# Kernel optimization log

Hardware: AMD Instinct MI355X
Metric: run time of the kernel (lower is better)

Reference implementation:

```python
import jax, jax.numpy as jnp
import numpy as np

N, E, H, NODE_IN, EDGE_DIM, L = 10000, 400000, 128, 6, 3, 4
LN_EPS = 1e-5


def _lin_init(key, fan_in, fan_out):
    return jax.random.normal(key, (fan_in, fan_out), dtype=jnp.float32) / np.sqrt(fan_in)


def setup_inputs() -> dict:
    key = jax.random.key(0)
    ks = jax.random.split(key, 24)
    x = jax.random.normal(ks[0], (N, NODE_IN), dtype=jnp.float32)
    edge_index = jax.random.randint(ks[1], (2, E), 0, N, dtype=jnp.int64)
    edge_attr = jax.random.normal(ks[2], (E, EDGE_DIM), dtype=jnp.float32)
    # encoder
    enc_w1 = _lin_init(ks[3], NODE_IN, H); enc_b1 = jnp.zeros((H,), jnp.float32)
    enc_w2 = _lin_init(ks[4], H, H); enc_b2 = jnp.zeros((H,), jnp.float32)
    # per-layer stacked params [L, ...]
    msg_w1 = jax.vmap(lambda k: _lin_init(k, 2 * H + EDGE_DIM, H))(jax.random.split(ks[5], L))
    msg_b1 = jnp.zeros((L, H), jnp.float32)
    msg_w2 = jax.vmap(lambda k: _lin_init(k, H, H))(jax.random.split(ks[6], L))
    msg_b2 = jnp.zeros((L, H), jnp.float32)
    upd_w1 = jax.vmap(lambda k: _lin_init(k, 2 * H, H))(jax.random.split(ks[7], L))
    upd_b1 = jnp.zeros((L, H), jnp.float32)
    upd_w2 = jax.vmap(lambda k: _lin_init(k, H, H))(jax.random.split(ks[8], L))
    upd_b2 = jnp.zeros((L, H), jnp.float32)
    ln_g = jnp.ones((L, H), jnp.float32)
    ln_b = jnp.zeros((L, H), jnp.float32)
    # decoder
    dec_w1 = _lin_init(ks[9], H, H); dec_b1 = jnp.zeros((H,), jnp.float32)
    dec_w2 = _lin_init(ks[10], H, 1); dec_b2 = jnp.zeros((1,), jnp.float32)
    return dict(x=x, edge_index=edge_index, edge_attr=edge_attr,
                enc_w1=enc_w1, enc_b1=enc_b1, enc_w2=enc_w2, enc_b2=enc_b2,
                msg_w1=msg_w1, msg_b1=msg_b1, msg_w2=msg_w2, msg_b2=msg_b2,
                upd_w1=upd_w1, upd_b1=upd_b1, upd_w2=upd_w2, upd_b2=upd_b2,
                ln_g=ln_g, ln_b=ln_b,
                dec_w1=dec_w1, dec_b1=dec_b1, dec_w2=dec_w2, dec_b2=dec_b2)


def _layernorm(h, g, b):
    mu = jnp.mean(h, axis=-1, keepdims=True)
    var = jnp.mean(jnp.square(h - mu), axis=-1, keepdims=True)
    return (h - mu) * jax.lax.rsqrt(var + LN_EPS) * g + b


def reference(x, edge_index, edge_attr,
              enc_w1, enc_b1, enc_w2, enc_b2,
              msg_w1, msg_b1, msg_w2, msg_b2,
              upd_w1, upd_b1, upd_w2, upd_b2,
              ln_g, ln_b,
              dec_w1, dec_b1, dec_w2, dec_b2):
    src, tgt = edge_index[0], edge_index[1]  # PyG default flow: message from x_j=src to x_i=tgt
    # in-degree counts for mean aggregation (zero-degree nodes -> 0 output, like scatter_mean)
    counts = jax.ops.segment_sum(jnp.ones((E,), jnp.float32), tgt, num_segments=N)
    inv_counts = (1.0 / jnp.maximum(counts, 1.0))[:, None]
    # encoder
    h = jax.nn.relu(x @ enc_w1 + enc_b1) @ enc_w2 + enc_b2  # [N, H]
    for l in range(L):
        x_i = h[tgt]  # [E, H] target features
        x_j = h[src]  # [E, H] source features
        m_in = jnp.concatenate([x_i, x_j, edge_attr], axis=-1)  # [E, 2H+edge_dim]
        m = jax.nn.relu(m_in @ msg_w1[l] + msg_b1[l]) @ msg_w2[l] + msg_b2[l]  # [E, H]
        agg = jax.ops.segment_sum(m, tgt, num_segments=N) * inv_counts  # [N, H] mean aggregate
        u_in = jnp.concatenate([h, agg], axis=-1)  # [N, 2H]
        u = jax.nn.relu(u_in @ upd_w1[l] + upd_b1[l]) @ upd_w2[l] + upd_b2[l]
        h = _layernorm(u + h, ln_g[l], ln_b[l])  # residual (in==out channels)
    # decoder
    return jax.nn.relu(h @ dec_w1 + dec_b1) @ dec_w2 + dec_b2  # [N, 1]
```

## Files before the change

kernel.cpp:

```cpp
#include <hip/hip_runtime.h>

#define NN 10000
#define NE 400000
#define HD 128
#define NIN 6
#define EDIM 3
#define NL 4
#define CAP 96
#define LN_EPS 1e-5f

typedef unsigned short u16;
using short8 = __attribute__((ext_vector_type(8))) short;
using f32x4 = __attribute__((ext_vector_type(4))) float;

__device__ __forceinline__ u16 f2bf(float x) {
    unsigned u = __float_as_uint(x);
    return (u16)((u + 0x7fff + ((u >> 16) & 1)) >> 16);
}
__device__ __forceinline__ float bf2f(u16 h) { return __uint_as_float(((unsigned)h) << 16); }
__device__ __forceinline__ void split2(float x, u16& hi, u16& lo) {
    hi = f2bf(x);
    lo = f2bf(x - bf2f(hi));
}
#define MFMA(a, b, c) __builtin_amdgcn_mfma_f32_16x16x32_bf16((a), (b), (c), 0, 0, 0)


__global__ __launch_bounds__(256) void k_prep(const float* __restrict__ msg_w2, const float* __restrict__ msg_b2,
                                              const float* __restrict__ upd_w1, float* __restrict__ M2,
                                              float* __restrict__ c2, int* __restrict__ cnt) {
    int idx = blockIdx.x * 256 + threadIdx.x;
    if (idx < 65536) {
        int l = idx >> 14, rem = idx & 16383, i = rem >> 7, jj = rem & 127;
        const float* U1b = upd_w1 + (size_t)l * 2 * HD * HD + (size_t)HD * HD;
        const float* W2 = msg_w2 + (size_t)l * HD * HD + (size_t)i * HD;
        float acc = 0.f;
        for (int t = 0; t < HD; ++t) acc += W2[t] * U1b[(size_t)t * HD + jj];
        M2[idx] = acc;
    } else if (idx < 66048) {
        int r = idx - 65536;
        int l = r >> 7, jj = r & 127;
        const float* U1b = upd_w1 + (size_t)l * 2 * HD * HD + (size_t)HD * HD;
        const float* b2 = msg_b2 + l * HD;
        float acc = 0.f;
        for (int t = 0; t < HD; ++t) acc += b2[t] * U1b[(size_t)t * HD + jj];
        c2[r] = acc;
    } else if (idx < 76048) {
        cnt[idx - 66048] = 0;
    }
}


__global__ __launch_bounds__(256) void k_frag(const float* __restrict__ upd_w1, const float* __restrict__ M2,
                                              const float* __restrict__ upd_w2, const float* __restrict__ msg_w1,
                                              const float* __restrict__ dec_w1, const float* __restrict__ enc_w2,
                                              u16* __restrict__ fG1, u16* __restrict__ fG2, u16* __restrict__ fPQ,
                                              u16* __restrict__ fDec, u16* __restrict__ fEnc) {
    int g = blockIdx.x * 256 + threadIdx.x;
    if (g < 16384) {
        int l = g >> 12, r = g & 4095;
        int ct = r >> 9, ks = (r >> 6) & 7, lane = r & 63;
        int n = ct * 16 + (lane & 15), kb = ks * 32 + ((lane >> 4) << 3);
        u16* dst = fG1 + (size_t)g * 8;
        const float* U = upd_w1 + (size_t)l * 256 * 128;
        const float* Ml = M2 + (size_t)l * 128 * 128;
#pragma unroll
        for (int j = 0; j < 8; ++j) {
            int k = kb + j;
            float v = (k < 128) ? U[(size_t)k * 128 + n] : Ml[(size_t)(k - 128) * 128 + n];
            dst[j] = f2bf(v);
        }
    } else if (g < 24576) {
        int gg = g - 16384;
        int l = gg >> 11, r = gg & 2047;
        int ct = r >> 8, ks = (r >> 6) & 3, lane = r & 63;
        int n = ct * 16 + (lane & 15), kb = ks * 32 + ((lane >> 4) << 3);
        u16* dst = fG2 + (size_t)gg * 8;
        const float* W = upd_w2 + (size_t)l * 128 * 128;
#pragma unroll
        for (int j = 0; j < 8; ++j) dst[j] = f2bf(W[(size_t)(kb + j) * 128 + n]);
    } else if (g < 40960) {
        int gg = g - 24576;
        int li = gg >> 12, r = gg & 4095;
        int ct = r >> 8, ks = (r >> 6) & 3, lane = r & 63;
        int n = ct * 16 + (lane & 15), kb = ks * 32 + ((lane >> 4) << 3);
        u16* dst = fPQ + (size_t)gg * 8;
        const float* W = msg_w1 + (size_t)li * (2 * HD + EDIM) * HD;
#pragma unroll
        for (int j = 0; j < 8; ++j) {
            int k = kb + j;
            float v = (n < 128) ? W[(size_t)k * 128 + n] : W[(size_t)(128 + k) * 128 + (n - 128)];
            dst[j] = f2bf(v);
        }
    } else if (g < 43008) {
        int r = g - 40960;
        int ct = r >> 8, ks = (r >> 6) & 3, lane = r & 63;
        int n = ct * 16 + (lane & 15), kb = ks * 32 + ((lane >> 4) << 3);
        u16* dst = fDec + (size_t)r * 8;
#pragma unroll
        for (int j = 0; j < 8; ++j) dst[j] = f2bf(dec_w1[(size_t)(kb + j) * 128 + n]);
    } else if (g < 45056) {
        int r = g - 43008;
        int ct = r >> 8, ks = (r >> 6) & 3, lane = r & 63;
        int n = ct * 16 + (lane & 15), kb = ks * 32 + ((lane >> 4) << 3);
        u16* dst = fEnc + (size_t)r * 8;
#pragma unroll
        for (int j = 0; j < 8; ++j) dst[j] = f2bf(enc_w2[(size_t)(kb + j) * 128 + n]);
    }
}


__global__ __launch_bounds__(256) void k_scatter(const int* __restrict__ src, const int* __restrict__ tgt,
                                                 const float* __restrict__ ea, int* __restrict__ cnt,
                                                 float4* __restrict__ sea) {
    int e = blockIdx.x * 256 + threadIdx.x;
    if (e >= NE) return;
    int t = tgt[e];
    int pos = atomicAdd(&cnt[t], 1);
    if (pos < CAP) {
        sea[t * CAP + pos] =
            make_float4(ea[e * 3], ea[e * 3 + 1], ea[e * 3 + 2], __uint_as_float((unsigned)src[e]));
    }
}


__global__ __launch_bounds__(512) void k_enc(const float* __restrict__ x, const float* __restrict__ ew1,
                                             const float* __restrict__ eb1, const u16* __restrict__ fEnc,
                                             const float* __restrict__ eb2, const u16* __restrict__ fPQ0,
                                             const float* __restrict__ mb1, u16* __restrict__ h_hi,
                                             u16* __restrict__ h_lo, float* __restrict__ PQf,
                                             u16* __restrict__ Qb) {
    __shared__ u16 tHi[2048], tLo[2048];
    int tid = threadIdx.x, w = tid >> 6, lane = tid & 63, q = lane >> 4, c = lane & 15;
    int band = blockIdx.x * 16;
    {
        int col = w * 16 + c;
        float wv[NIN];
#pragma unroll
        for (int k = 0; k < NIN; ++k) wv[k] = ew1[k * HD + col];
        float ebv = eb1[col];
#pragma unroll
        for (int reg = 0; reg < 4; ++reg) {
            int row = band + q * 4 + reg;
            float t = ebv;
#pragma unroll
            for (int k = 0; k < NIN; ++k) t += x[(size_t)row * NIN + k] * wv[k];
            t = fmaxf(t, 0.f);
            u16 hi, lo;
            split2(t, hi, lo);
            int r16 = q * 4 + reg;
            int a = r16 * 128 + (((col >> 3) ^ r16) << 3) + (col & 7);
            tHi[a] = hi;
            tLo[a] = lo;
        }
    }
    __syncthreads();
    short8 aH[4], aL[4];
#pragma unroll
    for (int ks = 0; ks < 4; ++ks) {
        int a = c * 128 + (((ks * 4 + q) ^ c) << 3);
        aH[ks] = *(const short8*)&tHi[a];
        aL[ks] = *(const short8*)&tLo[a];
    }
    f32x4 acc = {0, 0, 0, 0};
    {
        const u16* fb = fEnc + (size_t)w * 4 * 512 + lane * 8;
#pragma unroll
        for (int ks = 0; ks < 4; ++ks) {
            short8 b = *(const short8*)(fb + ks * 512);
            acc = MFMA(aH[ks], b, acc);
            acc = MFMA(aL[ks], b, acc);
        }
    }
    __syncthreads();
    {
        int col = w * 16 + c;
        float ebv = eb2[col];
#pragma unroll
        for (int reg = 0; reg < 4; ++reg) {
            int r16 = q * 4 + reg, row = band + r16;
            float hval = acc[reg] + ebv;
            u16 hi, lo;
            split2(hval, hi, lo);
            h_hi[(size_t)row * HD + col] = hi;
            h_lo[(size_t)row * HD + col] = lo;
            int a = r16 * 128 + (((col >> 3) ^ r16) << 3) + (col & 7);
            tHi[a] = hi;
            tLo[a] = lo;
        }
    }
    __syncthreads();
#pragma unroll
    for (int ks = 0; ks < 4; ++ks) {
        int a = c * 128 + (((ks * 4 + q) ^ c) << 3);
        aH[ks] = *(const short8*)&tHi[a];
        aL[ks] = *(const short8*)&tLo[a];
    }
#pragma unroll
    for (int i = 0; i < 2; ++i) {
        int ctg = w * 2 + i;
        const u16* fb = fPQ0 + (size_t)ctg * 4 * 512 + lane * 8;
        f32x4 a3 = {0, 0, 0, 0};
#pragma unroll
        for (int ks = 0; ks < 4; ++ks) {
            short8 b = *(const short8*)(fb + ks * 512);
            a3 = MFMA(aH[ks], b, a3);
            a3 = MFMA(aL[ks], b, a3);
        }
        int col = ctg * 16 + c;
        if (ctg < 8) {
            float bias = mb1[col];
#pragma unroll
            for (int reg = 0; reg < 4; ++reg)
                PQf[(size_t)(band + q * 4 + reg) * HD + col] = a3[reg] + bias;
        } else {
            int colq = col - 128;
#pragma unroll
            for (int reg = 0; reg < 4; ++reg)
                Qb[(size_t)(band + q * 4 + reg) * HD + colq] = f2bf(a3[reg]);
        }
    }
}


template <bool LAST>
__global__ __launch_bounds__(512) void k_layer(
    const float* __restrict__ PQf_in, const u16* __restrict__ Qb_in,
    const int* __restrict__ cnt, const float4* __restrict__ sea, const float* __restrict__ wc,
    u16* __restrict__ h_hi, u16* __restrict__ h_lo,
    const u16* __restrict__ fG1, const u16* __restrict__ fG2,
    const float* __restrict__ ub1, const float* __restrict__ c2l, const float* __restrict__ ub2,
    const float* __restrict__ g, const float* __restrict__ bb,
    const u16* __restrict__ fPQ, const float* __restrict__ nb1,
    float* __restrict__ PQf_out, u16* __restrict__ Qb_out,
    const u16* __restrict__ fDec, const float* __restrict__ db1, const float* __restrict__ dw2,
    const float* __restrict__ db2, float* __restrict__ out) {
    __shared__ u16 sHi[2048], sLo[2048];
    __shared__ u16 tHi[2048], tLo[2048];
    __shared__ float red[16][8][2];
    int tid = threadIdx.x, w = tid >> 6, lane = tid & 63, q = lane >> 4, c = lane & 15;
    int band = blockIdx.x * 16;
    int j = lane * 2;
    {
        float2 wcr0 = *(const float2*)(wc + j);
        float2 wcr1 = *(const float2*)(wc + HD + j);
        float2 wcr2 = *(const float2*)(wc + 2 * HD + j);
#pragma unroll
        for (int i = 0; i < 2; ++i) {
            int r16 = w * 2 + i;
            int n = __builtin_amdgcn_readfirstlane(band + r16);
            int cn = cnt[n];
            float invn = 1.0f / fmaxf((float)cn, 1.0f);
            int cle = __builtin_amdgcn_readfirstlane(cn < CAP ? cn : CAP);
            float2 p = *(const float2*)(PQf_in + (size_t)n * HD + j);
            float acc0 = 0.f, acc1 = 0.f;
            const float4* bucket = sea + (size_t)n * CAP;
            auto edge1 = [&](float4 A) {
                int sv = (int)__float_as_uint(A.w);
                float c0 = A.x * wcr0.x + A.y * wcr1.x + A.z * wcr2.x;
                float c1 = A.x * wcr0.y + A.y * wcr1.y + A.z * wcr2.y;
                unsigned u = *(const unsigned*)(Qb_in + (size_t)sv * HD + j);
                acc0 += fmaxf(p.x + __uint_as_float(u << 16) + c0, 0.f);
                acc1 += fmaxf(p.y + __uint_as_float(u & 0xffff0000u) + c1, 0.f);
            };
            int e = 0;
            for (; e + 3 < cle; e += 4) {
                float4 A0 = bucket[e], A1 = bucket[e + 1], A2 = bucket[e + 2], A3 = bucket[e + 3];
                edge1(A0);
                edge1(A1);
                edge1(A2);
                edge1(A3);
            }
            for (; e < cle; ++e) edge1(bucket[e]);
            float v0 = acc0 * invn, v1 = acc1 * invn;
            u16 h0, l0, h1, l1;
            split2(v0, h0, l0);
            split2(v1, h1, l1);
            int a = r16 * 128 + (((j >> 3) ^ r16) << 3) + (j & 7);
            *(ushort2*)&sHi[a] = make_ushort2(h0, h1);
            *(ushort2*)&sLo[a] = make_ushort2(l0, l1);
        }
    }
    __syncthreads();
    short8 aH[8], aL[8];
    {
        size_t rb = (size_t)(band + c) * HD + q * 8;
#pragma unroll
        for (int ks = 0; ks < 4; ++ks) {
            aH[ks] = *(const short8*)(h_hi + rb + ks * 32);
            aL[ks] = *(const short8*)(h_lo + rb + ks * 32);
            int a = c * 128 + (((ks * 4 + q) ^ c) << 3);
            aH[4 + ks] = *(const short8*)&sHi[a];
            aL[4 + ks] = *(const short8*)&sLo[a];
        }
    }
    f32x4 acc = {0, 0, 0, 0};
    {
        const u16* fb = fG1 + (size_t)w * 8 * 512 + lane * 8;
#pragma unroll
        for (int ks = 0; ks < 8; ++ks) {
            short8 b = *(const short8*)(fb + ks * 512);
            acc = MFMA(aH[ks], b, acc);
            acc = MFMA(aL[ks], b, acc);
        }
    }
    float alv[4];
#pragma unroll
    for (int reg = 0; reg < 4; ++reg) alv[reg] = (cnt[band + q * 4 + reg] > 0) ? 1.f : 0.f;
    {
        int col = w * 16 + c;
        float u1b = ub1[col], cc = c2l[col];
#pragma unroll
        for (int reg = 0; reg < 4; ++reg) {
            int r16 = q * 4 + reg;
            float t = fmaxf(acc[reg] + u1b + alv[reg] * cc, 0.f);
            u16 hi, lo;
            split2(t, hi, lo);
            int a = r16 * 128 + (((col >> 3) ^ r16) << 3) + (col & 7);
            tHi[a] = hi;
            tLo[a] = lo;
        }
    }
    __syncthreads();
    short8 aH2[4], aL2[4];
#pragma unroll
    for (int ks = 0; ks < 4; ++ks) {
        int a = c * 128 + (((ks * 4 + q) ^ c) << 3);
        aH2[ks] = *(const short8*)&tHi[a];
        aL2[ks] = *(const short8*)&tLo[a];
    }
    f32x4 acc2 = {0, 0, 0, 0};
    {
        const u16* fb = fG2 + (size_t)w * 4 * 512 + lane * 8;
#pragma unroll
        for (int ks = 0; ks < 4; ++ks) {
            short8 b = *(const short8*)(fb + ks * 512);
            acc2 = MFMA(aH2[ks], b, acc2);
            acc2 = MFMA(aL2[ks], b, acc2);
        }
    }
    float vv[4];
    {
        int col = w * 16 + c;
        float u2b = ub2[col];
#pragma unroll
        for (int reg = 0; reg < 4; ++reg) {
            size_t idx = (size_t)(band + q * 4 + reg) * HD + col;
            float hres = bf2f(h_hi[idx]) + bf2f(h_lo[idx]);
            vv[reg] = acc2[reg] + u2b + hres;
        }
    }
#pragma unroll
    for (int reg = 0; reg < 4; ++reg) {
        float s = vv[reg];
        float s2 = vv[reg] * vv[reg];
        for (int m = 1; m < 16; m <<= 1) {
            s += __shfl_xor(s, m);
            s2 += __shfl_xor(s2, m);
        }
        if (c == 0) {
            red[q * 4 + reg][w][0] = s;
            red[q * 4 + reg][w][1] = s2;
        }
    }
    __syncthreads();
    float mu[4], rs[4];
#pragma unroll
    for (int reg = 0; reg < 4; ++reg) {
        int r16 = q * 4 + reg;
        float S1 = 0.f, S2 = 0.f;
#pragma unroll
        for (int ww = 0; ww < 8; ++ww) {
            S1 += red[r16][ww][0];
            S2 += red[r16][ww][1];
        }
        float m = S1 * (1.f / HD);
        float var = S2 * (1.f / HD) - m * m;
        mu[reg] = m;
        rs[reg] = rsqrtf(var + LN_EPS);
    }
    {
        int col = w * 16 + c;
        float gg = g[col], bv = bb[col];
#pragma unroll
        for (int reg = 0; reg < 4; ++reg) {
            int r16 = q * 4 + reg;
            float o = (vv[reg] - mu[reg]) * rs[reg] * gg + bv;
            u16 hi, lo;
            split2(o, hi, lo);
            int a = r16 * 128 + (((col >> 3) ^ r16) << 3) + (col & 7);
            tHi[a] = hi;
            tLo[a] = lo;
            if (!LAST) {
                size_t idx = (size_t)(band + r16) * HD + col;
                h_hi[idx] = hi;
                h_lo[idx] = lo;
            }
        }
    }
    __syncthreads();
    short8 aH3[4], aL3[4];
#pragma unroll
    for (int ks = 0; ks < 4; ++ks) {
        int a = c * 128 + (((ks * 4 + q) ^ c) << 3);
        aH3[ks] = *(const short8*)&tHi[a];
        aL3[ks] = *(const short8*)&tLo[a];
    }
    if (!LAST) {
#pragma unroll
        for (int i = 0; i < 2; ++i) {
            int ctg = w * 2 + i;
            const u16* fb = fPQ + (size_t)ctg * 4 * 512 + lane * 8;
            f32x4 a3 = {0, 0, 0, 0};
#pragma unroll
            for (int ks = 0; ks < 4; ++ks) {
                short8 b = *(const short8*)(fb + ks * 512);
                a3 = MFMA(aH3[ks], b, a3);
                a3 = MFMA(aL3[ks], b, a3);
            }
            int col = ctg * 16 + c;
            if (ctg < 8) {
                float bias = nb1[col];
#pragma unroll
                for (int reg = 0; reg < 4; ++reg)
                    PQf_out[(size_t)(band + q * 4 + reg) * HD + col] = a3[reg] + bias;
            } else {
                int colq = col - 128;
#pragma unroll
                for (int reg = 0; reg < 4; ++reg)
                    Qb_out[(size_t)(band + q * 4 + reg) * HD + colq] = f2bf(a3[reg]);
            }
        }
    } else {
        float part[4];
        {
            const u16* fb = fDec + (size_t)w * 4 * 512 + lane * 8;
            f32x4 a3 = {0, 0, 0, 0};
#pragma unroll
            for (int ks = 0; ks < 4; ++ks) {
                short8 b = *(const short8*)(fb + ks * 512);
                a3 = MFMA(aH3[ks], b, a3);
                a3 = MFMA(aL3[ks], b, a3);
            }
            int col = w * 16 + c;
            float w2v = dw2[col], b1v = db1[col];
#pragma unroll
            for (int reg = 0; reg < 4; ++reg) part[reg] = fmaxf(a3[reg] + b1v, 0.f) * w2v;
        }
#pragma unroll
        for (int reg = 0; reg < 4; ++reg) {
            float s = part[reg];
            for (int m = 1; m < 16; m <<= 1) s += __shfl_xor(s, m);
            if (c == 0) red[q * 4 + reg][w][0] = s;
        }
        __syncthreads();
        if (tid < 16) {
            float s = db2[0];
#pragma unroll
            for (int ww = 0; ww < 8; ++ww) s += red[tid][ww][0];
            out[band + tid] = s;
        }
    }
}


extern "C" void kernel_launch(void* const* d_in, const int* in_sizes, int n_in,
                              void* d_out, int out_size, void* d_ws, size_t ws_size,
                              hipStream_t stream) {
    const float* x = (const float*)d_in[0];
    const int* eidx = (const int*)d_in[1];
    const float* eattr = (const float*)d_in[2];
    const float* enc_w1 = (const float*)d_in[3];
    const float* enc_b1 = (const float*)d_in[4];
    const float* enc_w2 = (const float*)d_in[5];
    const float* enc_b2 = (const float*)d_in[6];
    const float* msg_w1 = (const float*)d_in[7];
    const float* msg_b1 = (const float*)d_in[8];
    const float* msg_w2 = (const float*)d_in[9];
    const float* msg_b2 = (const float*)d_in[10];
    const float* upd_w1 = (const float*)d_in[11];
    const float* upd_b1 = (const float*)d_in[12];
    const float* upd_w2 = (const float*)d_in[13];
    const float* upd_b2 = (const float*)d_in[14];
    const float* ln_g = (const float*)d_in[15];
    const float* ln_b = (const float*)d_in[16];
    const float* dec_w1 = (const float*)d_in[17];
    const float* dec_b1 = (const float*)d_in[18];
    const float* dec_w2 = (const float*)d_in[19];
    const float* dec_b2 = (const float*)d_in[20];
    const int* srcp = eidx;
    const int* tgtp = eidx + NE;

    char* base = (char*)d_ws;
    size_t off = 0;
    auto alloc = [&](size_t bytes) -> void* {
        off = (off + 15) & ~(size_t)15;
        void* p = base + off;
        off += bytes;
        return p;
    };
    float4* sea = (float4*)alloc((size_t)NN * CAP * 16);
    float* PQf0 = (float*)alloc((size_t)NN * HD * 4);
    float* PQf1 = (float*)alloc((size_t)NN * HD * 4);
    u16* Qb0 = (u16*)alloc((size_t)NN * HD * 2);
    u16* Qb1 = (u16*)alloc((size_t)NN * HD * 2);
    u16* h_hi = (u16*)alloc((size_t)NN * HD * 2);
    u16* h_lo = (u16*)alloc((size_t)NN * HD * 2);
    int* cnt = (int*)alloc((size_t)NN * 4);
    float* M2 = (float*)alloc((size_t)NL * HD * HD * 4);
    float* c2 = (float*)alloc((size_t)NL * HD * 4);
    u16* fG1 = (u16*)alloc((size_t)131072 * 2);
    u16* fG2 = (u16*)alloc((size_t)65536 * 2);
    u16* fPQ = (u16*)alloc((size_t)131072 * 2);
    u16* fDec = (u16*)alloc((size_t)16384 * 2);
    u16* fEnc = (u16*)alloc((size_t)16384 * 2);

    k_prep<<<298, 256, 0, stream>>>(msg_w2, msg_b2, upd_w1, M2, c2, cnt);
    k_frag<<<176, 256, 0, stream>>>(upd_w1, M2, upd_w2, msg_w1, dec_w1, enc_w2, fG1, fG2, fPQ, fDec, fEnc);
    k_scatter<<<(NE + 255) / 256, 256, 0, stream>>>(srcp, tgtp, eattr, cnt, sea);
    k_enc<<<NN / 16, 512, 0, stream>>>(x, enc_w1, enc_b1, fEnc, enc_b2, fPQ, msg_b1, h_hi, h_lo, PQf0, Qb0);

    float* PQin = PQf0;
    u16* Qin = Qb0;
    float* PQout = PQf1;
    u16* Qout = Qb1;
    for (int l = 0; l < NL; ++l) {
        const float* wc = msg_w1 + (size_t)l * (2 * HD + EDIM) * HD + (size_t)2 * HD * HD;
        if (l < NL - 1) {
            k_layer<false><<<NN / 16, 512, 0, stream>>>(
                PQin, Qin, cnt, sea, wc, h_hi, h_lo,
                fG1 + (size_t)l * 32768, fG2 + (size_t)l * 16384,
                upd_b1 + l * HD, c2 + l * HD, upd_b2 + l * HD, ln_g + l * HD, ln_b + l * HD,
                fPQ + (size_t)(l + 1) * 32768, msg_b1 + (size_t)(l + 1) * HD, PQout, Qout,
                nullptr, nullptr, nullptr, nullptr, nullptr);
        } else {
            k_layer<true><<<NN / 16, 512, 0, stream>>>(
                PQin, Qin, cnt, sea, wc, h_hi, h_lo,
                fG1 + (size_t)l * 32768, fG2 + (size_t)l * 16384,
                upd_b1 + l * HD, c2 + l * HD, upd_b2 + l * HD, ln_g + l * HD, ln_b + l * HD,
                nullptr, nullptr, nullptr, nullptr,
                fDec, dec_b1, dec_w2, dec_b2, (float*)d_out);
        }
        float* tf = PQin; PQin = PQout; PQout = tf;
        u16* tq = Qin; Qin = Qout; Qout = tq;
    }
}
```

Before: 286.5 us.

## Fuse all stages into one persistent cooperative kernel with grid syncs

Replaces the chain of prep, fragment, scatter, encoder and four layer launches with a single cooperative kernel of 625 blocks that separates stages with grid.sync(). The aim is to remove per-launch overhead and the gaps between the many small kernels. The layer body also streams MFMA A operands instead of holding them all in registers, which lowers register pressure so six blocks per CU can be co-resident, as the cooperative launch needs. A multi-kernel fallback is kept if the cooperative launch fails. Grid-wide barriers add their own sync cost, and the lower register cap may cause spills.

```diff
diff --git a/kernel.cpp b/kernel.cpp
--- a/kernel.cpp
+++ b/kernel.cpp
@@ -1,4 +1,7 @@
 #include <hip/hip_runtime.h>
+#include <hip/hip_cooperative_groups.h>
+
+namespace cg = cooperative_groups;
 
 #define NN 10000
 #define NE 400000
@@ -8,6 +11,9 @@
 #define NL 4
 #define CAP 96
 #define LN_EPS 1e-5f
+#define GRID_C 625
+#define NTHR 512
+#define TOTTHR (GRID_C * NTHR)
 
 typedef unsigned short u16;
 using short8 = __attribute__((ext_vector_type(8))) short;
@@ -25,10 +31,10 @@
 #define MFMA(a, b, c) __builtin_amdgcn_mfma_f32_16x16x32_bf16((a), (b), (c), 0, 0, 0)
 
 
-__global__ __launch_bounds__(256) void k_prep(const float* __restrict__ msg_w2, const float* __restrict__ msg_b2,
-                                              const float* __restrict__ upd_w1, float* __restrict__ M2,
-                                              float* __restrict__ c2, int* __restrict__ cnt) {
-    int idx = blockIdx.x * 256 + threadIdx.x;
+__device__ __forceinline__ void prep_item(
+    int idx, const float* msg_w2, const float* msg_b2, const float* upd_w1, const float* upd_w2,
+    const float* msg_w1, const float* dec_w1, const float* enc_w2, float* M2, float* c2, int* cnt,
+    u16* fG2, u16* fPQ, u16* fDec, u16* fEnc) {
     if (idx < 65536) {
         int l = idx >> 14, rem = idx & 16383, i = rem >> 7, jj = rem & 127;
         const float* U1b = upd_w1 + (size_t)l * 2 * HD * HD + (size_t)HD * HD;
@@ -46,43 +52,20 @@
         c2[r] = acc;
     } else if (idx < 76048) {
         cnt[idx - 66048] = 0;
-    }
-}
-
-
-__global__ __launch_bounds__(256) void k_frag(const float* __restrict__ upd_w1, const float* __restrict__ M2,
-                                              const float* __restrict__ upd_w2, const float* __restrict__ msg_w1,
-                                              const float* __restrict__ dec_w1, const float* __restrict__ enc_w2,
-                                              u16* __restrict__ fG1, u16* __restrict__ fG2, u16* __restrict__ fPQ,
-                                              u16* __restrict__ fDec, u16* __restrict__ fEnc) {
-    int g = blockIdx.x * 256 + threadIdx.x;
-    if (g < 16384) {
-        int l = g >> 12, r = g & 4095;
-        int ct = r >> 9, ks = (r >> 6) & 7, lane = r & 63;
-        int n = ct * 16 + (lane & 15), kb = ks * 32 + ((lane >> 4) << 3);
-        u16* dst = fG1 + (size_t)g * 8;
-        const float* U = upd_w1 + (size_t)l * 256 * 128;
-        const float* Ml = M2 + (size_t)l * 128 * 128;
-#pragma unroll
-        for (int j = 0; j < 8; ++j) {
-            int k = kb + j;
-            float v = (k < 128) ? U[(size_t)k * 128 + n] : Ml[(size_t)(k - 128) * 128 + n];
-            dst[j] = f2bf(v);
-        }
-    } else if (g < 24576) {
-        int gg = g - 16384;
+    } else if (idx < 84240) {
+        int gg = idx - 76048;
         int l = gg >> 11, r = gg & 2047;
-        int ct = r >> 8, ks = (r >> 6) & 3, lane = r & 63;
-        int n = ct * 16 + (lane & 15), kb = ks * 32 + ((lane >> 4) << 3);
+        int ct = r >> 8, ks = (r >> 6) & 3, ln = r & 63;
+        int n = ct * 16 + (ln & 15), kb = ks * 32 + ((ln >> 4) << 3);
         u16* dst = fG2 + (size_t)gg * 8;
         const float* W = upd_w2 + (size_t)l * 128 * 128;
 #pragma unroll
         for (int j = 0; j < 8; ++j) dst[j] = f2bf(W[(size_t)(kb + j) * 128 + n]);
-    } else if (g < 40960) {
-        int gg = g - 24576;
+    } else if (idx < 100624) {
+        int gg = idx - 84240;
         int li = gg >> 12, r = gg & 4095;
-        int ct = r >> 8, ks = (r >> 6) & 3, lane = r & 63;
-        int n = ct * 16 + (lane & 15), kb = ks * 32 + ((lane >> 4) << 3);
+        int ct = r >> 8, ks = (r >> 6) & 3, ln = r & 63;
+        int n = ct * 16 + (ln & 15), kb = ks * 32 + ((ln >> 4) << 3);
         u16* dst = fPQ + (size_t)gg * 8;
         const float* W = msg_w1 + (size_t)li * (2 * HD + EDIM) * HD;
 #pragma unroll
@@ -91,47 +74,43 @@
             float v = (n < 128) ? W[(size_t)k * 128 + n] : W[(size_t)(128 + k) * 128 + (n - 128)];
             dst[j] = f2bf(v);
         }
-    } else if (g < 43008) {
-        int r = g - 40960;
-        int ct = r >> 8, ks = (r >> 6) & 3, lane = r & 63;
-        int n = ct * 16 + (lane & 15), kb = ks * 32 + ((lane >> 4) << 3);
+    } else if (idx < 102672) {
+        int r = idx - 100624;
+        int ct = r >> 8, ks = (r >> 6) & 3, ln = r & 63;
+        int n = ct * 16 + (ln & 15), kb = ks * 32 + ((ln >> 4) << 3);
         u16* dst = fDec + (size_t)r * 8;
 #pragma unroll
         for (int j = 0; j < 8; ++j) dst[j] = f2bf(dec_w1[(size_t)(kb + j) * 128 + n]);
-    } else if (g < 45056) {
-        int r = g - 43008;
-        int ct = r >> 8, ks = (r >> 6) & 3, lane = r & 63;
-        int n = ct * 16 + (lane & 15), kb = ks * 32 + ((lane >> 4) << 3);
+    } else if (idx < 104720) {
+        int r = idx - 102672;
+        int ct = r >> 8, ks = (r >> 6) & 3, ln = r & 63;
+        int n = ct * 16 + (ln & 15), kb = ks * 32 + ((ln >> 4) << 3);
         u16* dst = fEnc + (size_t)r * 8;
 #pragma unroll
         for (int j = 0; j < 8; ++j) dst[j] = f2bf(enc_w2[(size_t)(kb + j) * 128 + n]);
     }
 }
 
-
-__global__ __launch_bounds__(256) void k_scatter(const int* __restrict__ src, const int* __restrict__ tgt,
-                                                 const float* __restrict__ ea, int* __restrict__ cnt,
-                                                 float4* __restrict__ sea) {
-    int e = blockIdx.x * 256 + threadIdx.x;
-    if (e >= NE) return;
-    int t = tgt[e];
-    int pos = atomicAdd(&cnt[t], 1);
-    if (pos < CAP) {
-        sea[t * CAP + pos] =
-            make_float4(ea[e * 3], ea[e * 3 + 1], ea[e * 3 + 2], __uint_as_float((unsigned)src[e]));
-    }
-}
-
-
-__global__ __launch_bounds__(512) void k_enc(const float* __restrict__ x, const float* __restrict__ ew1,
-                                             const float* __restrict__ eb1, const u16* __restrict__ fEnc,
-                                             const float* __restrict__ eb2, const u16* __restrict__ fPQ0,
-                                             const float* __restrict__ mb1, u16* __restrict__ h_hi,
-                                             u16* __restrict__ h_lo, float* __restrict__ PQf,
-                                             u16* __restrict__ Qb) {
-    __shared__ u16 tHi[2048], tLo[2048];
-    int tid = threadIdx.x, w = tid >> 6, lane = tid & 63, q = lane >> 4, c = lane & 15;
-    int band = blockIdx.x * 16;
+__device__ __forceinline__ void fg1_item(int g, const float* upd_w1, const float* M2, u16* fG1) {
+    int l = g >> 12, r = g & 4095;
+    int ct = r >> 9, ks = (r >> 6) & 7, ln = r & 63;
+    int n = ct * 16 + (ln & 15), kb = ks * 32 + ((ln >> 4) << 3);
+    u16* dst = fG1 + (size_t)g * 8;
+    const float* U = upd_w1 + (size_t)l * 256 * 128;
+    const float* Ml = M2 + (size_t)l * 128 * 128;
+#pragma unroll
+    for (int j = 0; j < 8; ++j) {
+        int k = kb + j;
+        float v = (k < 128) ? U[(size_t)k * 128 + n] : Ml[(size_t)(k - 128) * 128 + n];
+        dst[j] = f2bf(v);
+    }
+}
+
+__device__ __forceinline__ void enc_body(
+    int band, int tid, const float* x, const float* ew1, const float* eb1, const u16* fEnc,
+    const float* eb2, const u16* fPQ0, const float* mb1, u16* h_hi, u16* h_lo, float* PQf, u16* Qb,
+    u16* tHi, u16* tLo) {
+    int w = tid >> 6, lane = tid & 63, q = lane >> 4, c = lane & 15;
     {
         int col = w * 16 + c;
         float wv[NIN];
@@ -221,24 +200,14 @@
     }
 }
 
-
-template <bool LAST>
-__global__ __launch_bounds__(512) void k_layer(
-    const float* __restrict__ PQf_in, const u16* __restrict__ Qb_in,
-    const int* __restrict__ cnt, const float4* __restrict__ sea, const float* __restrict__ wc,
-    u16* __restrict__ h_hi, u16* __restrict__ h_lo,
-    const u16* __restrict__ fG1, const u16* __restrict__ fG2,
-    const float* __restrict__ ub1, const float* __restrict__ c2l, const float* __restrict__ ub2,
-    const float* __restrict__ g, const float* __restrict__ bb,
-    const u16* __restrict__ fPQ, const float* __restrict__ nb1,
-    float* __restrict__ PQf_out, u16* __restrict__ Qb_out,
-    const u16* __restrict__ fDec, const float* __restrict__ db1, const float* __restrict__ dw2,
-    const float* __restrict__ db2, float* __restrict__ out) {
-    __shared__ u16 sHi[2048], sLo[2048];
-    __shared__ u16 tHi[2048], tLo[2048];
-    __shared__ float red[16][8][2];
-    int tid = threadIdx.x, w = tid >> 6, lane = tid & 63, q = lane >> 4, c = lane & 15;
-    int band = blockIdx.x * 16;
+__device__ __forceinline__ void layer_body(
+    int band, int tid, bool LAST, const float* PQin, const u16* Qin, const int* cnt,
+    const float4* sea, const float* wc, u16* h_hi, u16* h_lo, const u16* fG1l, const u16* fG2l,
+    const float* ub1, const float* c2l, const float* ub2, const float* g, const float* bb,
+    const u16* fPQn, const float* nb1, float* PQout, u16* Qout, const u16* fDec, const float* db1,
+    const float* dw2, const float* db2, float* out, u16* sHi, u16* sLo, u16* tHi, u16* tLo,
+    float (*red)[8][2]) {
+    int w = tid >> 6, lane = tid & 63, q = lane >> 4, c = lane & 15;
     int j = lane * 2;
     {
         float2 wcr0 = *(const float2*)(wc + j);
@@ -251,14 +220,14 @@
             int cn = cnt[n];
             float invn = 1.0f / fmaxf((float)cn, 1.0f);
             int cle = __builtin_amdgcn_readfirstlane(cn < CAP ? cn : CAP);
-            float2 p = *(const float2*)(PQf_in + (size_t)n * HD + j);
+            float2 p = *(const float2*)(PQin + (size_t)n * HD + j);
             float acc0 = 0.f, acc1 = 0.f;
             const float4* bucket = sea + (size_t)n * CAP;
-            auto edge1 = [&](float4 A) {
-                int sv = (int)__float_as_uint(A.w);
-                float c0 = A.x * wcr0.x + A.y * wcr1.x + A.z * wcr2.x;
-                float c1 = A.x * wcr0.y + A.y * wcr1.y + A.z * wcr2.y;
-                unsigned u = *(const unsigned*)(Qb_in + (size_t)sv * HD + j);
+            auto edge1 = [&](float4 Av) {
+                int sv = (int)__float_as_uint(Av.w);
+                float c0 = Av.x * wcr0.x + Av.y * wcr1.x + Av.z * wcr2.x;
+                float c1 = Av.x * wcr0.y + Av.y * wcr1.y + Av.z * wcr2.y;
+                unsigned u = *(const unsigned*)(Qin + (size_t)sv * HD + j);
                 acc0 += fmaxf(p.x + __uint_as_float(u << 16) + c0, 0.f);
                 acc1 += fmaxf(p.y + __uint_as_float(u & 0xffff0000u) + c1, 0.f);
             };
@@ -281,26 +250,30 @@
         }
     }
     __syncthreads();
-    short8 aH[8], aL[8];
-    {
+    f32x4 acc = {0, 0, 0, 0};
+    {
+        const u16* fb = fG1l + (size_t)w * 8 * 512 + lane * 8;
         size_t rb = (size_t)(band + c) * HD + q * 8;
+        short8 hH[4], hL[4];
 #pragma unroll
         for (int ks = 0; ks < 4; ++ks) {
-            aH[ks] = *(const short8*)(h_hi + rb + ks * 32);
-            aL[ks] = *(const short8*)(h_lo + rb + ks * 32);
+            hH[ks] = *(const short8*)(h_hi + rb + ks * 32);
+            hL[ks] = *(const short8*)(h_lo + rb + ks * 32);
+        }
+#pragma unroll
+        for (int ks = 0; ks < 4; ++ks) {
+            short8 b = *(const short8*)(fb + ks * 512);
+            acc = MFMA(hH[ks], b, acc);
+            acc = MFMA(hL[ks], b, acc);
+        }
+#pragma unroll
+        for (int ks = 0; ks < 4; ++ks) {
             int a = c * 128 + (((ks * 4 + q) ^ c) << 3);
-            aH[4 + ks] = *(const short8*)&sHi[a];
-            aL[4 + ks] = *(const short8*)&sLo[a];
-        }
-    }
-    f32x4 acc = {0, 0, 0, 0};
-    {
-        const u16* fb = fG1 + (size_t)w * 8 * 512 + lane * 8;
-#pragma unroll
-        for (int ks = 0; ks < 8; ++ks) {
-            short8 b = *(const short8*)(fb + ks * 512);
-            acc = MFMA(aH[ks], b, acc);
-            acc = MFMA(aL[ks], b, acc);
+            short8 sH = *(const short8*)&sHi[a];
+            short8 sL = *(const short8*)&sLo[a];
+            short8 b = *(const short8*)(fb + (4 + ks) * 512);
+            acc = MFMA(sH, b, acc);
+            acc = MFMA(sL, b, acc);
         }
     }
     float alv[4];
@@ -321,21 +294,17 @@
         }
     }
     __syncthreads();
-    short8 aH2[4], aL2[4];
-#pragma unroll
-    for (int ks = 0; ks < 4; ++ks) {
-        int a = c * 128 + (((ks * 4 + q) ^ c) << 3);
-        aH2[ks] = *(const short8*)&tHi[a];
-        aL2[ks] = *(const short8*)&tLo[a];
-    }
     f32x4 acc2 = {0, 0, 0, 0};
     {
-        const u16* fb = fG2 + (size_t)w * 4 * 512 + lane * 8;
+        const u16* fb = fG2l + (size_t)w * 4 * 512 + lane * 8;
 #pragma unroll
         for (int ks = 0; ks < 4; ++ks) {
+            int a = c * 128 + (((ks * 4 + q) ^ c) << 3);
+            short8 aHh = *(const short8*)&tHi[a];
+            short8 aLl = *(const short8*)&tLo[a];
             short8 b = *(const short8*)(fb + ks * 512);
-            acc2 = MFMA(aH2[ks], b, acc2);
-            acc2 = MFMA(aL2[ks], b, acc2);
+            acc2 = MFMA(aHh, b, acc2);
+            acc2 = MFMA(aLl, b, acc2);
         }
     }
     float vv[4];
@@ -409,7 +378,7 @@
 #pragma unroll
         for (int i = 0; i < 2; ++i) {
             int ctg = w * 2 + i;
-            const u16* fb = fPQ + (size_t)ctg * 4 * 512 + lane * 8;
+            const u16* fb = fPQn + (size_t)ctg * 4 * 512 + lane * 8;
             f32x4 a3 = {0, 0, 0, 0};
 #pragma unroll
             for (int ks = 0; ks < 4; ++ks) {
@@ -422,12 +391,12 @@
                 float bias = nb1[col];
 #pragma unroll
                 for (int reg = 0; reg < 4; ++reg)
-                    PQf_out[(size_t)(band + q * 4 + reg) * HD + col] = a3[reg] + bias;
+                    PQout[(size_t)(band + q * 4 + reg) * HD + col] = a3[reg] + bias;
             } else {
                 int colq = col - 128;
 #pragma unroll
                 for (int reg = 0; reg < 4; ++reg)
-                    Qb_out[(size_t)(band + q * 4 + reg) * HD + colq] = f2bf(a3[reg]);
+                    Qout[(size_t)(band + q * 4 + reg) * HD + colq] = f2bf(a3[reg]);
             }
         }
     } else {
@@ -463,33 +432,159 @@
 }
 
 
+struct MegaArgs {
+    const float* x;
+    const int* srcp;
+    const int* tgtp;
+    const float* eattr;
+    const float* enc_w1;
+    const float* enc_b1;
+    const float* enc_w2;
+    const float* enc_b2;
+    const float* msg_w1;
+    const float* msg_b1;
+    const float* msg_w2;
+    const float* msg_b2;
+    const float* upd_w1;
+    const float* upd_b1;
+    const float* upd_w2;
+    const float* upd_b2;
+    const float* ln_g;
+    const float* ln_b;
+    const float* dec_w1;
+    const float* dec_b1;
+    const float* dec_w2;
+    const float* dec_b2;
+    float* out;
+    float4* sea;
+    float* PQf0;
+    float* PQf1;
+    u16* Qb0;
+    u16* Qb1;
+    u16* h_hi;
+    u16* h_lo;
+    int* cnt;
+    float* M2;
+    float* c2;
+    u16* fG1;
+    u16* fG2;
+    u16* fPQ;
+    u16* fDec;
+    u16* fEnc;
+};
+
+
+__global__ __launch_bounds__(NTHR, 6) void k_mega(MegaArgs A) {
+    cg::grid_group grid = cg::this_grid();
+    __shared__ u16 sHi[2048], sLo[2048];
+    __shared__ u16 tHi[2048], tLo[2048];
+    __shared__ float red[16][8][2];
+    int tid = threadIdx.x;
+    int band = blockIdx.x * 16;
+    int gid = blockIdx.x * NTHR + tid;
+
+    prep_item(gid, A.msg_w2, A.msg_b2, A.upd_w1, A.upd_w2, A.msg_w1, A.dec_w1, A.enc_w2, A.M2, A.c2,
+              A.cnt, A.fG2, A.fPQ, A.fDec, A.fEnc);
+    grid.sync();
+    if (gid < 16384) fg1_item(gid, A.upd_w1, A.M2, A.fG1);
+    for (int e = gid; e < NE; e += TOTTHR) {
+        int t = A.tgtp[e];
+        int pos = atomicAdd(&A.cnt[t], 1);
+        if (pos < CAP) {
+            A.sea[t * CAP + pos] = make_float4(A.eattr[e * 3], A.eattr[e * 3 + 1], A.eattr[e * 3 + 2],
+                                               __uint_as_float((unsigned)A.srcp[e]));
+        }
+    }
+    enc_body(band, tid, A.x, A.enc_w1, A.enc_b1, A.fEnc, A.enc_b2, A.fPQ, A.msg_b1, A.h_hi, A.h_lo,
+             A.PQf0, A.Qb0, tHi, tLo);
+    grid.sync();
+    const float* PQin = A.PQf0;
+    const u16* Qin = A.Qb0;
+    float* PQout = A.PQf1;
+    u16* Qout = A.Qb1;
+    for (int l = 0; l < NL; ++l) {
+        bool LAST = (l == NL - 1);
+        layer_body(band, tid, LAST, PQin, Qin, A.cnt, A.sea,
+                   A.msg_w1 + (size_t)l * (2 * HD + EDIM) * HD + (size_t)2 * HD * HD, A.h_hi, A.h_lo,
+                   A.fG1 + (size_t)l * 32768, A.fG2 + (size_t)l * 16384, A.upd_b1 + l * HD,
+                   A.c2 + l * HD, A.upd_b2 + l * HD, A.ln_g + l * HD, A.ln_b + l * HD,
+                   LAST ? nullptr : (A.fPQ + (size_t)(l + 1) * 32768),
+                   LAST ? nullptr : (A.msg_b1 + (size_t)(l + 1) * HD), PQout, Qout, A.fDec, A.dec_b1,
+                   A.dec_w2, A.dec_b2, A.out, sHi, sLo, tHi, tLo, red);
+        if (!LAST) {
+            grid.sync();
+            const float* tp = PQin;
+            PQin = PQout;
+            PQout = (float*)tp;
+            const u16* tq = Qin;
+            Qin = Qout;
+            Qout = (u16*)tq;
+        }
+    }
+}
+
+
+__global__ __launch_bounds__(256) void k_prep(
+    const float* __restrict__ msg_w2, const float* __restrict__ msg_b2, const float* __restrict__ upd_w1,
+    const float* __restrict__ upd_w2, const float* __restrict__ msg_w1, const float* __restrict__ dec_w1,
+    const float* __restrict__ enc_w2, float* __restrict__ M2, float* __restrict__ c2, int* __restrict__ cnt,
+    u16* __restrict__ fG2, u16* __restrict__ fPQ, u16* __restrict__ fDec, u16* __restrict__ fEnc) {
+    int idx = blockIdx.x * 256 + threadIdx.x;
+    prep_item(idx, msg_w2, msg_b2, upd_w1, upd_w2, msg_w1, dec_w1, enc_w2, M2, c2, cnt, fG2, fPQ,
+              fDec, fEnc);
+}
+
+__global__ __launch_bounds__(256) void k_scatfrag(
+    const int* __restrict__ src, const int* __restrict__ tgt, const float* __restrict__ ea,
+    int* __restrict__ cnt, float4* __restrict__ sea, const float* __restrict__ upd_w1,
+    const float* __restrict__ M2, u16* __restrict__ fG1) {
+    if (blockIdx.x < 64) {
+        fg1_item(blockIdx.x * 256 + threadIdx.x, upd_w1, M2, fG1);
+    } else {
+        int e = (blockIdx.x - 64) * 256 + threadIdx.x;
+        if (e >= NE) return;
+        int t = tgt[e];
+        int pos = atomicAdd(&cnt[t], 1);
+        if (pos < CAP) {
+            sea[t * CAP + pos] =
+                make_float4(ea[e * 3], ea[e * 3 + 1], ea[e * 3 + 2], __uint_as_float((unsigned)src[e]));
+        }
+    }
+}
+
+__global__ __launch_bounds__(512) void k_enc(const float* __restrict__ x, const float* __restrict__ ew1,
+                                             const float* __restrict__ eb1, const u16* __restrict__ fEnc,
+                                             const float* __restrict__ eb2, const u16* __restrict__ fPQ0,
+                                             const float* __restrict__ mb1, u16* __restrict__ h_hi,
+                                             u16* __restrict__ h_lo, float* __restrict__ PQf,
+                                             u16* __restrict__ Qb) {
+    __shared__ u16 tHi[2048], tLo[2048];
+    enc_body(blockIdx.x * 16, threadIdx.x, x, ew1, eb1, fEnc, eb2, fPQ0, mb1, h_hi, h_lo, PQf, Qb,
+             tHi, tLo);
+}
+
+template <bool LAST>
+__global__ __launch_bounds__(512) void k_layer(
+    const float* __restrict__ PQf_in, const u16* __restrict__ Qb_in, const int* __restrict__ cnt,
+    const float4* __restrict__ sea, const float* __restrict__ wc, u16* __restrict__ h_hi,
+    u16* __restrict__ h_lo, const u16* __restrict__ fG1, const u16* __restrict__ fG2,
+    const float* __restrict__ ub1, const float* __restrict__ c2l, const float* __restrict__ ub2,
+    const float* __restrict__ g, const float* __restrict__ bb, const u16* __restrict__ fPQ,
+    const float* __restrict__ nb1, float* __restrict__ PQf_out, u16* __restrict__ Qb_out,
+    const u16* __restrict__ fDec, const float* __restrict__ db1, const float* __restrict__ dw2,
+    const float* __restrict__ db2, float* __restrict__ out) {
+    __shared__ u16 sHi[2048], sLo[2048];
+    __shared__ u16 tHi[2048], tLo[2048];
+    __shared__ float red[16][8][2];
+    layer_body(blockIdx.x * 16, threadIdx.x, LAST, PQf_in, Qb_in, cnt, sea, wc, h_hi, h_lo, fG1, fG2,
+               ub1, c2l, ub2, g, bb, fPQ, nb1, PQf_out, Qb_out, fDec, db1, dw2, db2, out, sHi, sLo,
+               tHi, tLo, red);
+}
+
+
 extern "C" void kernel_launch(void* const* d_in, const int* in_sizes, int n_in,
                               void* d_out, int out_size, void* d_ws, size_t ws_size,
                               hipStream_t stream) {
-    const float* x = (const float*)d_in[0];
-    const int* eidx = (const int*)d_in[1];
-    const float* eattr = (const float*)d_in[2];
-    const float* enc_w1 = (const float*)d_in[3];
-    const float* enc_b1 = (const float*)d_in[4];
-    const float* enc_w2 = (const float*)d_in[5];
-    const float* enc_b2 = (const float*)d_in[6];
-    const float* msg_w1 = (const float*)d_in[7];
-    const float* msg_b1 = (const float*)d_in[8];
-    const float* msg_w2 = (const float*)d_in[9];
-    const float* msg_b2 = (const float*)d_in[10];
-    const float* upd_w1 = (const float*)d_in[11];
-    const float* upd_b1 = (const float*)d_in[12];
-    const float* upd_w2 = (const float*)d_in[13];
-    const float* upd_b2 = (const float*)d_in[14];
-    const float* ln_g = (const float*)d_in[15];
-    const float* ln_b = (const float*)d_in[16];
-    const float* dec_w1 = (const float*)d_in[17];
-    const float* dec_b1 = (const float*)d_in[18];
-    const float* dec_w2 = (const float*)d_in[19];
-    const float* dec_b2 = (const float*)d_in[20];
-    const int* srcp = eidx;
-    const int* tgtp = eidx + NE;
-
     char* base = (char*)d_ws;
     size_t off = 0;
     auto alloc = [&](size_t bytes) -> void* {
@@ -498,49 +593,84 @@
         off += bytes;
         return p;
     };
-    float4* sea = (float4*)alloc((size_t)NN * CAP * 16);
-    float* PQf0 = (float*)alloc((size_t)NN * HD * 4);
-    float* PQf1 = (float*)alloc((size_t)NN * HD * 4);
-    u16* Qb0 = (u16*)alloc((size_t)NN * HD * 2);
-    u16* Qb1 = (u16*)alloc((size_t)NN * HD * 2);
-    u16* h_hi = (u16*)alloc((size_t)NN * HD * 2);
-    u16* h_lo = (u16*)alloc((size_t)NN * HD * 2);
-    int* cnt = (int*)alloc((size_t)NN * 4);
-    float* M2 = (float*)alloc((size_t)NL * HD * HD * 4);
-    float* c2 = (float*)alloc((size_t)NL * HD * 4);
-    u16* fG1 = (u16*)alloc((size_t)131072 * 2);
-    u16* fG2 = (u16*)alloc((size_t)65536 * 2);
-    u16* fPQ = (u16*)alloc((size_t)131072 * 2);
-    u16* fDec = (u16*)alloc((size_t)16384 * 2);
-    u16* fEnc = (u16*)alloc((size_t)16384 * 2);
-
-    k_prep<<<298, 256, 0, stream>>>(msg_w2, msg_b2, upd_w1, M2, c2, cnt);
-    k_frag<<<176, 256, 0, stream>>>(upd_w1, M2, upd_w2, msg_w1, dec_w1, enc_w2, fG1, fG2, fPQ, fDec, fEnc);
-    k_scatter<<<(NE + 255) / 256, 256, 0, stream>>>(srcp, tgtp, eattr, cnt, sea);
-    k_enc<<<NN / 16, 512, 0, stream>>>(x, enc_w1, enc_b1, fEnc, enc_b2, fPQ, msg_b1, h_hi, h_lo, PQf0, Qb0);
-
-    float* PQin = PQf0;
-    u16* Qin = Qb0;
-    float* PQout = PQf1;
-    u16* Qout = Qb1;
-    for (int l = 0; l < NL; ++l) {
-        const float* wc = msg_w1 + (size_t)l * (2 * HD + EDIM) * HD + (size_t)2 * HD * HD;
-        if (l < NL - 1) {
-            k_layer<false><<<NN / 16, 512, 0, stream>>>(
-                PQin, Qin, cnt, sea, wc, h_hi, h_lo,
-                fG1 + (size_t)l * 32768, fG2 + (size_t)l * 16384,
-                upd_b1 + l * HD, c2 + l * HD, upd_b2 + l * HD, ln_g + l * HD, ln_b + l * HD,
-                fPQ + (size_t)(l + 1) * 32768, msg_b1 + (size_t)(l + 1) * HD, PQout, Qout,
-                nullptr, nullptr, nullptr, nullptr, nullptr);
-        } else {
-            k_layer<true><<<NN / 16, 512, 0, stream>>>(
-                PQin, Qin, cnt, sea, wc, h_hi, h_lo,
-                fG1 + (size_t)l * 32768, fG2 + (size_t)l * 16384,
-                upd_b1 + l * HD, c2 + l * HD, upd_b2 + l * HD, ln_g + l * HD, ln_b + l * HD,
-                nullptr, nullptr, nullptr, nullptr,
-                fDec, dec_b1, dec_w2, dec_b2, (float*)d_out);
-        }
-        float* tf = PQin; PQin = PQout; PQout = tf;
-        u16* tq = Qin; Qin = Qout; Qout = tq;
-    }
-}
+    MegaArgs A;
+    A.x = (const float*)d_in[0];
+    const int* eidx = (const int*)d_in[1];
+    A.srcp = eidx;
+    A.tgtp = eidx + NE;
+    A.eattr = (const float*)d_in[2];
+    A.enc_w1 = (const float*)d_in[3];
+    A.enc_b1 = (const float*)d_in[4];
+    A.enc_w2 = (const float*)d_in[5];
+    A.enc_b2 = (const float*)d_in[6];
+    A.msg_w1 = (const float*)d_in[7];
+    A.msg_b1 = (const float*)d_in[8];
+    A.msg_w2 = (const float*)d_in[9];
+    A.msg_b2 = (const float*)d_in[10];
+    A.upd_w1 = (const float*)d_in[11];
+    A.upd_b1 = (const float*)d_in[12];
+    A.upd_w2 = (const float*)d_in[13];
+    A.upd_b2 = (const float*)d_in[14];
+    A.ln_g = (const float*)d_in[15];
+    A.ln_b = (const float*)d_in[16];
+    A.dec_w1 = (const float*)d_in[17];
+    A.dec_b1 = (const float*)d_in[18];
+    A.dec_w2 = (const float*)d_in[19];
+    A.dec_b2 = (const float*)d_in[20];
+    A.out = (float*)d_out;
+    A.sea = (float4*)alloc((size_t)NN * CAP * 16);
+    A.PQf0 = (float*)alloc((size_t)NN * HD * 4);
+    A.PQf1 = (float*)alloc((size_t)NN * HD * 4);
+    A.Qb0 = (u16*)alloc((size_t)NN * HD * 2);
+    A.Qb1 = (u16*)alloc((size_t)NN * HD * 2);
+    A.h_hi = (u16*)alloc((size_t)NN * HD * 2);
+    A.h_lo = (u16*)alloc((size_t)NN * HD * 2);
+    A.cnt = (int*)alloc((size_t)NN * 4);
+    A.M2 = (float*)alloc((size_t)NL * HD * HD * 4);
+    A.c2 = (float*)alloc((size_t)NL * HD * 4);
+    A.fG1 = (u16*)alloc((size_t)131072 * 2);
+    A.fG2 = (u16*)alloc((size_t)65536 * 2);
+    A.fPQ = (u16*)alloc((size_t)131072 * 2);
+    A.fDec = (u16*)alloc((size_t)16384 * 2);
+    A.fEnc = (u16*)alloc((size_t)16384 * 2);
+
+    void* kargs[] = {&A};
+    hipError_t err =
+        hipLaunchCooperativeKernel((void*)k_mega, dim3(GRID_C), dim3(NTHR), kargs, 0, stream);
+    if (err != hipSuccess) {
+        (void)hipGetLastError();
+        k_prep<<<410, 256, 0, stream>>>(A.msg_w2, A.msg_b2, A.upd_w1, A.upd_w2, A.msg_w1, A.dec_w1,
+                                        A.enc_w2, A.M2, A.c2, A.cnt, A.fG2, A.fPQ, A.fDec, A.fEnc);
+        k_scatfrag<<<64 + (NE + 255) / 256, 256, 0, stream>>>(A.srcp, A.tgtp, A.eattr, A.cnt, A.sea,
+                                                              A.upd_w1, A.M2, A.fG1);
+        k_enc<<<NN / 16, 512, 0, stream>>>(A.x, A.enc_w1, A.enc_b1, A.fEnc, A.enc_b2, A.fPQ,
+                                           A.msg_b1, A.h_hi, A.h_lo, A.PQf0, A.Qb0);
+        float* PQin = A.PQf0;
+        u16* Qin = A.Qb0;
+        float* PQout = A.PQf1;
+        u16* Qout = A.Qb1;
+        for (int l = 0; l < NL; ++l) {
+            const float* wc = A.msg_w1 + (size_t)l * (2 * HD + EDIM) * HD + (size_t)2 * HD * HD;
+            if (l < NL - 1) {
+                k_layer<false><<<NN / 16, 512, 0, stream>>>(
+                    PQin, Qin, A.cnt, A.sea, wc, A.h_hi, A.h_lo, A.fG1 + (size_t)l * 32768,
+                    A.fG2 + (size_t)l * 16384, A.upd_b1 + l * HD, A.c2 + l * HD, A.upd_b2 + l * HD,
+                    A.ln_g + l * HD, A.ln_b + l * HD, A.fPQ + (size_t)(l + 1) * 32768,
+                    A.msg_b1 + (size_t)(l + 1) * HD, PQout, Qout, nullptr, nullptr, nullptr, nullptr,
+                    nullptr);
+            } else {
+                k_layer<true><<<NN / 16, 512, 0, stream>>>(
+                    PQin, Qin, A.cnt, A.sea, wc, A.h_hi, A.h_lo, A.fG1 + (size_t)l * 32768,
+                    A.fG2 + (size_t)l * 16384, A.upd_b1 + l * HD, A.c2 + l * HD, A.upd_b2 + l * HD,
+                    A.ln_g + l * HD, A.ln_b + l * HD, nullptr, nullptr, nullptr, nullptr, A.fDec,
+                    A.dec_b1, A.dec_w2, A.dec_b2, A.out);
+            }
+            float* tf = PQin;
+            PQin = PQout;
+            PQout = tf;
+            u16* tq = Qin;
+            Qin = Qout;
+            Qout = tq;
+        }
+    }
+}
```

New measurement: 873.2 us. +204.8%, slower.
